# Optimization experiments

Hardware: AMD Instinct MI355X
Metric: run time of the kernel (lower is better)

Reference implementation:

```python
import jax, jax.numpy as jnp
import numpy as np

INPUT_SIZE = 4
HIDDEN_SIZE = 64
OUTPUT_SIZE = 40
BATCH = 4096
SEQ_LEN = 512


def setup_inputs() -> dict:
    key = jax.random.key(0)
    ks = jax.random.split(key, 7)
    s_ih = 1.0 / np.sqrt(HIDDEN_SIZE)
    x = jax.random.normal(ks[0], (BATCH, SEQ_LEN, INPUT_SIZE), dtype=jnp.float32)
    # PyTorch nn.RNN params, uniform(-1/sqrt(H), 1/sqrt(H))
    W_ih = jax.random.uniform(ks[1], (HIDDEN_SIZE, INPUT_SIZE), minval=-s_ih, maxval=s_ih, dtype=jnp.float32)
    W_hh = jax.random.uniform(ks[2], (HIDDEN_SIZE, HIDDEN_SIZE), minval=-s_ih, maxval=s_ih, dtype=jnp.float32)
    b_ih = jax.random.uniform(ks[3], (HIDDEN_SIZE,), minval=-s_ih, maxval=s_ih, dtype=jnp.float32)
    b_hh = jax.random.uniform(ks[4], (HIDDEN_SIZE,), minval=-s_ih, maxval=s_ih, dtype=jnp.float32)
    fc_W = jax.random.uniform(ks[5], (OUTPUT_SIZE, HIDDEN_SIZE), minval=-s_ih, maxval=s_ih, dtype=jnp.float32)
    fc_b = jax.random.uniform(ks[6], (OUTPUT_SIZE,), minval=-s_ih, maxval=s_ih, dtype=jnp.float32)
    return {"x": x, "W_ih": W_ih, "W_hh": W_hh, "b_ih": b_ih, "b_hh": b_hh, "fc_W": fc_W, "fc_b": fc_b}


def reference(x, W_ih, W_hh, b_ih, b_hh, fc_W, fc_b):
    B = x.shape[0]
    # Precompute input projections for all timesteps: [T, B, H]
    xp = jnp.einsum('bti,hi->tbh', x, W_ih) + (b_ih + b_hh)

    def step(h, xp_t):
        h = jnp.tanh(xp_t + h @ W_hh.T)
        return h, None

    h0 = jnp.zeros((B, HIDDEN_SIZE), dtype=x.dtype)
    h_last, _ = jax.lax.scan(step, h0, xp)
    # fc on last timestep hidden state
    return h_last @ fc_W.T + fc_b
```

## Files before the change

kernel.cpp:

```cpp
#include <hip/hip_runtime.h>
#include <math.h>

#define BATCH 4096
#define SEQ_T 512
#define ISZ   4
#define HID   64
#define OSZ   40
#define RPB   16

typedef __attribute__((ext_vector_type(8))) _Float16     half8;
typedef __attribute__((ext_vector_type(2))) _Float16     half2v;
typedef __attribute__((ext_vector_type(4))) float        float4v;
typedef __attribute__((ext_vector_type(2))) unsigned int uint2v;

static __device__ __forceinline__ half2v pk_f16(float a, float b) {
    return __builtin_bit_cast(half2v, __builtin_amdgcn_cvt_pkrtz(a, b));
}

static __device__ __forceinline__ float fast_tanh(float x) {
    float e = __expf(2.0f * x);
    return 1.0f - 2.0f * __builtin_amdgcn_rcpf(e + 1.0f);
}

__global__ __launch_bounds__(256, 1)
void rnn_f16x2_kernel(const float* __restrict__ x,
                      const float* __restrict__ W_ih,
                      const float* __restrict__ W_hh,
                      const float* __restrict__ b_ih,
                      const float* __restrict__ b_hh,
                      const float* __restrict__ fc_W,
                      const float* __restrict__ fc_b,
                      float* __restrict__ out)
{
    __shared__ __attribute__((aligned(16))) _Float16 hterm[2][2][8][16][8];
    __shared__ __attribute__((aligned(16))) float hf[16][68];

    const int tid  = threadIdx.x;
    const int wv   = tid >> 6;
    const int lane = tid & 63;
    const int n    = lane & 15;
    const int q    = lane >> 4;
    const int blk0 = blockIdx.x * RPB;

    {
        unsigned int* p = (unsigned int*)hterm;
        #pragma unroll
        for (int i = tid; i < (int)(sizeof(hterm) / 4); i += 256) p[i] = 0u;
    }

    half8 A10, A11, A20, A21;
    {
        const float* wr = W_hh + (16 * wv + n) * HID;
        #pragma unroll
        for (int j = 0; j < 8; ++j) {
            float f0 = wr[     8 * q + j];
            float f1 = wr[32 + 8 * q + j];
            _Float16 h0 = (_Float16)f0; A10[j] = h0; A20[j] = (_Float16)(f0 - (float)h0);
            _Float16 h1 = (_Float16)f1; A11[j] = h1; A21[j] = (_Float16)(f1 - (float)h1);
        }
    }

    const int r0 = 16 * wv + 4 * q;
    float wih[4][4], bias[4];
    #pragma unroll
    for (int r = 0; r < 4; ++r) {
        bias[r] = b_ih[r0 + r] + b_hh[r0 + r];
        #pragma unroll
        for (int i = 0; i < ISZ; ++i) wih[r][i] = W_ih[(r0 + r) * ISZ + i];
    }

    const float* xrow = x + (size_t)(blk0 + n) * SEQ_T * ISZ;
    float4v xcur = *(const float4v*)(xrow);
    float4v xnxt = *(const float4v*)(xrow + ISZ);

    const int gw = 2 * wv + (q >> 1);
    const int j0 = 4 * (q & 1);

    float hl0 = 0.f, hl1 = 0.f, hl2 = 0.f, hl3 = 0.f;

    __syncthreads();

#define MFMA16(A, B, C) __builtin_amdgcn_mfma_f32_16x16x32_f16((A), (B), (C), 0, 0, 0)
#define RNN_STEP(RB, WB, T)                                                    \
    {                                                                          \
        int tn = (T) + 2; if (tn > SEQ_T - 1) tn = SEQ_T - 1;                  \
        const float4v xf = *(const float4v*)(xrow + (size_t)tn * ISZ);         \
        half8 B10 = *(const half8*)&hterm[RB][0][    q][n][0];                 \
        half8 B11 = *(const half8*)&hterm[RB][0][4 + q][n][0];                 \
        half8 B20 = *(const half8*)&hterm[RB][1][    q][n][0];                 \
        half8 B21 = *(const half8*)&hterm[RB][1][4 + q][n][0];                 \
        float p0 = bias[0], p1 = bias[1], p2 = bias[2], p3 = bias[3];          \
        _Pragma("unroll")                                                      \
        for (int i = 0; i < ISZ; ++i) {                                        \
            p0 = fmaf(xcur[i], wih[0][i], p0);                                 \
            p1 = fmaf(xcur[i], wih[1][i], p1);                                 \
            p2 = fmaf(xcur[i], wih[2][i], p2);                                 \
            p3 = fmaf(xcur[i], wih[3][i], p3);                                 \
        }                                                                      \
        float4v accA = {p0, p1, p2, p3};                                       \
        float4v accB = {0.f, 0.f, 0.f, 0.f};                                   \
        accA = MFMA16(A10, B10, accA);  accB = MFMA16(A11, B11, accB);         \
        accA = MFMA16(A10, B20, accA);  accB = MFMA16(A11, B21, accB);         \
        accA = MFMA16(A20, B10, accA);  accB = MFMA16(A21, B11, accB);         \
        hl0 = fast_tanh(accA[0] + accB[0]); hl1 = fast_tanh(accA[1] + accB[1]);\
        hl2 = fast_tanh(accA[2] + accB[2]); hl3 = fast_tanh(accA[3] + accB[3]);\
        half2v hi01 = pk_f16(hl0, hl1), hi23 = pk_f16(hl2, hl3);               \
        float s0 = hl0 - (float)hi01[0], s1 = hl1 - (float)hi01[1];            \
        float s2 = hl2 - (float)hi23[0], s3 = hl3 - (float)hi23[1];            \
        half2v lo01 = pk_f16(s0, s1), lo23 = pk_f16(s2, s3);                   \
        uint2v whi = { __builtin_bit_cast(unsigned int, hi01),                 \
                       __builtin_bit_cast(unsigned int, hi23) };               \
        uint2v wlo = { __builtin_bit_cast(unsigned int, lo01),                 \
                       __builtin_bit_cast(unsigned int, lo23) };               \
        *(uint2v*)&hterm[WB][0][gw][n][j0] = whi;                              \
        *(uint2v*)&hterm[WB][1][gw][n][j0] = wlo;                              \
        xcur = xnxt; xnxt = xf;                                                \
        __syncthreads();                                                       \
    }

    for (int t = 0; t < SEQ_T; t += 2) {
        RNN_STEP(0, 1, t)
        RNN_STEP(1, 0, t + 1)
    }
#undef RNN_STEP
#undef MFMA16

    {
        float4v hv = {hl0, hl1, hl2, hl3};
        *(float4v*)&hf[n][16 * wv + 4 * q] = hv;
    }
    __syncthreads();
    for (int it = tid; it < RPB * OSZ; it += 256) {
        const int b = it / OSZ;
        const int o = it - b * OSZ;
        const float* wo = fc_W + o * HID;
        float acc = fc_b[o];
        #pragma unroll
        for (int j = 0; j < HID; ++j)
            acc = fmaf(hf[b][j], wo[j], acc);
        out[(size_t)(blk0 + b) * OSZ + o] = acc;
    }
}

extern "C" void kernel_launch(void* const* d_in, const int* in_sizes, int n_in,
                              void* d_out, int out_size, void* d_ws, size_t ws_size,
                              hipStream_t stream) {
    const float* x    = (const float*)d_in[0];
    const float* W_ih = (const float*)d_in[1];
    const float* W_hh = (const float*)d_in[2];
    const float* b_ih = (const float*)d_in[3];
    const float* b_hh = (const float*)d_in[4];
    const float* fc_W = (const float*)d_in[5];
    const float* fc_b = (const float*)d_in[6];
    float* out = (float*)d_out;

    rnn_f16x2_kernel<<<BATCH / RPB, 256, 0, stream>>>(
        x, W_ih, W_hh, b_ih, b_hh, fc_W, fc_b, out);
}
```

Measured before the change: 230.8 us.

## Use two waves per block and fold input projection into an MFMA

The block shrinks from four waves to two, so each wave computes 32 hidden rows (two 16-row tiles) per timestep. This halves the number of waves taking part in each per-step barrier. The input projection plus bias, previously done with scalar FMAs, now runs as an extra MFMA on split-f16 operands of x, W_ih and the bias. In exchange each wave issues twice as many MFMAs per step on a serial chain, and the block fills fewer SIMDs, which may lengthen the critical path.

```diff
diff --git a/kernel.cpp b/kernel.cpp
--- a/kernel.cpp
+++ b/kernel.cpp
@@ -12,25 +12,25 @@
 typedef __attribute__((ext_vector_type(2))) _Float16     half2v;
 typedef __attribute__((ext_vector_type(4))) float        float4v;
 typedef __attribute__((ext_vector_type(2))) unsigned int uint2v;
+typedef __attribute__((ext_vector_type(4))) unsigned int uint4v;
 
 static __device__ __forceinline__ half2v pk_f16(float a, float b) {
     return __builtin_bit_cast(half2v, __builtin_amdgcn_cvt_pkrtz(a, b));
 }
-
 static __device__ __forceinline__ float fast_tanh(float x) {
     float e = __expf(2.0f * x);
     return 1.0f - 2.0f * __builtin_amdgcn_rcpf(e + 1.0f);
 }
 
-__global__ __launch_bounds__(256, 1)
-void rnn_f16x2_kernel(const float* __restrict__ x,
-                      const float* __restrict__ W_ih,
-                      const float* __restrict__ W_hh,
-                      const float* __restrict__ b_ih,
-                      const float* __restrict__ b_hh,
-                      const float* __restrict__ fc_W,
-                      const float* __restrict__ fc_b,
-                      float* __restrict__ out)
+__global__ __launch_bounds__(128, 1)
+void rnn_w2_kernel(const float* __restrict__ x,
+                   const float* __restrict__ W_ih,
+                   const float* __restrict__ W_hh,
+                   const float* __restrict__ b_ih,
+                   const float* __restrict__ b_hh,
+                   const float* __restrict__ fc_W,
+                   const float* __restrict__ fc_b,
+                   float* __restrict__ out)
 {
     __shared__ __attribute__((aligned(16))) _Float16 hterm[2][2][8][16][8];
     __shared__ __attribute__((aligned(16))) float hf[16][68];
@@ -41,42 +41,50 @@
     const int n    = lane & 15;
     const int q    = lane >> 4;
     const int blk0 = blockIdx.x * RPB;
+    const int j0   = 4 * (q & 1);
 
     {
         unsigned int* p = (unsigned int*)hterm;
         #pragma unroll
-        for (int i = tid; i < (int)(sizeof(hterm) / 4); i += 256) p[i] = 0u;
+        for (int i = tid; i < (int)(sizeof(hterm) / 4); i += 128) p[i] = 0u;
     }
 
-    half8 A10, A11, A20, A21;
-    {
-        const float* wr = W_hh + (16 * wv + n) * HID;
+    half8 A1c0[2], A1c1[2], A2c0[2], A2c1[2], A3[2];
+    #pragma unroll
+    for (int s = 0; s < 2; ++s) {
+        const int row = 32 * wv + 16 * s + n;
+        const float* wr = W_hh + row * HID;
         #pragma unroll
         for (int j = 0; j < 8; ++j) {
             float f0 = wr[     8 * q + j];
             float f1 = wr[32 + 8 * q + j];
-            _Float16 h0 = (_Float16)f0; A10[j] = h0; A20[j] = (_Float16)(f0 - (float)h0);
-            _Float16 h1 = (_Float16)f1; A11[j] = h1; A21[j] = (_Float16)(f1 - (float)h1);
+            _Float16 h0 = (_Float16)f0; A1c0[s][j] = h0; A2c0[s][j] = (_Float16)(f0 - (float)h0);
+            _Float16 h1 = (_Float16)f1; A1c1[s][j] = h1; A2c1[s][j] = (_Float16)(f1 - (float)h1);
         }
-    }
-
-    const int r0 = 16 * wv + 4 * q;
-    float wih[4][4], bias[4];
-    #pragma unroll
-    for (int r = 0; r < 4; ++r) {
-        bias[r] = b_ih[r0 + r] + b_hh[r0 + r];
+        float wf0 = W_ih[row * 4 + 0], wf1 = W_ih[row * 4 + 1];
+        float wf2 = W_ih[row * 4 + 2], wf3 = W_ih[row * 4 + 3];
+        float bs  = b_ih[row] + b_hh[row];
+        _Float16 bh = (_Float16)bs;
+        _Float16 bl = (_Float16)(bs - (float)bh);
         #pragma unroll
-        for (int i = 0; i < ISZ; ++i) wih[r][i] = W_ih[(r0 + r) * ISZ + i];
+        for (int j = 0; j < 8; ++j) {
+            float w = (j&3)==0 ? wf0 : (j&3)==1 ? wf1 : (j&3)==2 ? wf2 : wf3;
+            _Float16 whi = (_Float16)w;
+            _Float16 wlo = (_Float16)(w - (float)whi);
+            _Float16 v = (_Float16)0.0f;
+            if (q == 0) v = whi;
+            else if (q == 1) v = (j < 4) ? wlo : (j == 4) ? bh : (j == 5) ? bl : (_Float16)0.0f;
+            A3[s][j] = v;
+        }
     }
 
     const float* xrow = x + (size_t)(blk0 + n) * SEQ_T * ISZ;
     float4v xcur = *(const float4v*)(xrow);
     float4v xnxt = *(const float4v*)(xrow + ISZ);
 
-    const int gw = 2 * wv + (q >> 1);
-    const int j0 = 4 * (q & 1);
+    float hl[2][4] = {{0.f,0.f,0.f,0.f},{0.f,0.f,0.f,0.f}};
 
-    float hl0 = 0.f, hl1 = 0.f, hl2 = 0.f, hl3 = 0.f;
+    const unsigned int ONE2 = 0x3C003C00u;
 
     __syncthreads();
 
@@ -89,31 +97,48 @@
         half8 B11 = *(const half8*)&hterm[RB][0][4 + q][n][0];                 \
         half8 B20 = *(const half8*)&hterm[RB][1][    q][n][0];                 \
         half8 B21 = *(const half8*)&hterm[RB][1][4 + q][n][0];                 \
-        float p0 = bias[0], p1 = bias[1], p2 = bias[2], p3 = bias[3];          \
+                              \
+        half2v xh01 = pk_f16(xcur[0], xcur[1]), xh23 = pk_f16(xcur[2], xcur[3]); \
+        float l0 = xcur[0] - (float)xh01[0], l1 = xcur[1] - (float)xh01[1];    \
+        float l2 = xcur[2] - (float)xh23[0], l3 = xcur[3] - (float)xh23[1];    \
+        half2v xl01 = pk_f16(l0, l1), xl23 = pk_f16(l2, l3);                   \
+        unsigned int uh01 = __builtin_bit_cast(unsigned int, xh01);            \
+        unsigned int uh23 = __builtin_bit_cast(unsigned int, xh23);            \
+        unsigned int ul01 = __builtin_bit_cast(unsigned int, xl01);            \
+        unsigned int ul23 = __builtin_bit_cast(unsigned int, xl23);            \
+        uint4v bt = { (q < 2) ? uh01 : 0u,                                     \
+                      (q < 2) ? uh23 : 0u,                                     \
+                      (q == 0) ? ul01 : (q == 1) ? ONE2 : 0u,                  \
+                      (q == 0) ? ul23 : 0u };                                  \
+        half8 B3 = __builtin_bit_cast(half8, bt);                              \
         _Pragma("unroll")                                                      \
-        for (int i = 0; i < ISZ; ++i) {                                        \
-            p0 = fmaf(xcur[i], wih[0][i], p0);                                 \
-            p1 = fmaf(xcur[i], wih[1][i], p1);                                 \
-            p2 = fmaf(xcur[i], wih[2][i], p2);                                 \
-            p3 = fmaf(xcur[i], wih[3][i], p3);                                 \
+        for (int s = 0; s < 2; ++s) {                                          \
+            float4v accA = {0.f, 0.f, 0.f, 0.f};                               \
+            float4v accB = {0.f, 0.f, 0.f, 0.f};                               \
+            accB = MFMA16(A3[s],   B3,  accB);                                 \
+            accA = MFMA16(A1c0[s], B10, accA);                                 \
+            accB = MFMA16(A1c1[s], B11, accB);                                 \
+            accA = MFMA16(A1c0[s], B20, accA);                                 \
+            accB = MFMA16(A1c1[s], B21, accB);                                 \
+            accA = MFMA16(A2c0[s], B10, accA);                                 \
+            accB = MFMA16(A2c1[s], B11, accB);                                 \
+            hl[s][0] = fast_tanh(accA[0] + accB[0]);                           \
+            hl[s][1] = fast_tanh(accA[1] + accB[1]);                           \
+            hl[s][2] = fast_tanh(accA[2] + accB[2]);                           \
+            hl[s][3] = fast_tanh(accA[3] + accB[3]);                           \
+            half2v hi01 = pk_f16(hl[s][0], hl[s][1]);                          \
+            half2v hi23 = pk_f16(hl[s][2], hl[s][3]);                          \
+            float s0 = hl[s][0] - (float)hi01[0], s1 = hl[s][1] - (float)hi01[1]; \
+            float s2 = hl[s][2] - (float)hi23[0], s3 = hl[s][3] - (float)hi23[1]; \
+            half2v lo01 = pk_f16(s0, s1), lo23 = pk_f16(s2, s3);               \
+            uint2v whi = { __builtin_bit_cast(unsigned int, hi01),             \
+                           __builtin_bit_cast(unsigned int, hi23) };           \
+            uint2v wlo = { __builtin_bit_cast(unsigned int, lo01),             \
+                           __builtin_bit_cast(unsigned int, lo23) };           \
+            const int g = 4 * wv + 2 * s + (q >> 1);                           \
+            *(uint2v*)&hterm[WB][0][g][n][j0] = whi;                           \
+            *(uint2v*)&hterm[WB][1][g][n][j0] = wlo;                           \
         }                                                                      \
-        float4v accA = {p0, p1, p2, p3};                                       \
-        float4v accB = {0.f, 0.f, 0.f, 0.f};                                   \
-        accA = MFMA16(A10, B10, accA);  accB = MFMA16(A11, B11, accB);         \
-        accA = MFMA16(A10, B20, accA);  accB = MFMA16(A11, B21, accB);         \
-        accA = MFMA16(A20, B10, accA);  accB = MFMA16(A21, B11, accB);         \
-        hl0 = fast_tanh(accA[0] + accB[0]); hl1 = fast_tanh(accA[1] + accB[1]);\
-        hl2 = fast_tanh(accA[2] + accB[2]); hl3 = fast_tanh(accA[3] + accB[3]);\
-        half2v hi01 = pk_f16(hl0, hl1), hi23 = pk_f16(hl2, hl3);               \
-        float s0 = hl0 - (float)hi01[0], s1 = hl1 - (float)hi01[1];            \
-        float s2 = hl2 - (float)hi23[0], s3 = hl3 - (float)hi23[1];            \
-        half2v lo01 = pk_f16(s0, s1), lo23 = pk_f16(s2, s3);                   \
-        uint2v whi = { __builtin_bit_cast(unsigned int, hi01),                 \
-                       __builtin_bit_cast(unsigned int, hi23) };               \
-        uint2v wlo = { __builtin_bit_cast(unsigned int, lo01),                 \
-                       __builtin_bit_cast(unsigned int, lo23) };               \
-        *(uint2v*)&hterm[WB][0][gw][n][j0] = whi;                              \
-        *(uint2v*)&hterm[WB][1][gw][n][j0] = wlo;                              \
         xcur = xnxt; xnxt = xf;                                                \
         __syncthreads();                                                       \
     }
@@ -125,12 +150,13 @@
 #undef RNN_STEP
 #undef MFMA16
 
-    {
-        float4v hv = {hl0, hl1, hl2, hl3};
-        *(float4v*)&hf[n][16 * wv + 4 * q] = hv;
+    #pragma unroll
+    for (int s = 0; s < 2; ++s) {
+        float4v hv = {hl[s][0], hl[s][1], hl[s][2], hl[s][3]};
+        *(float4v*)&hf[n][32 * wv + 16 * s + 4 * q] = hv;
     }
     __syncthreads();
-    for (int it = tid; it < RPB * OSZ; it += 256) {
+    for (int it = tid; it < RPB * OSZ; it += 128) {
         const int b = it / OSZ;
         const int o = it - b * OSZ;
         const float* wo = fc_W + o * HID;
@@ -154,6 +180,6 @@
     const float* fc_b = (const float*)d_in[6];
     float* out = (float*)d_out;
 
-    rnn_f16x2_kernel<<<BATCH / RPB, 256, 0, stream>>>(
+    rnn_w2_kernel<<<BATCH / RPB, 128, 0, stream>>>(
         x, W_ih, W_hh, b_ih, b_hh, fc_W, fc_b, out);
 }
```

After: 301.9 us. +30.8%, slower.
